# Kernel tuning notes

Hardware: AMD Instinct MI355X
Metric: run time of the kernel (lower is better)

## Reference

```python
import jax, jax.numpy as jnp
import numpy as np

B, T = 1, 1024
V, C, H, L = 50304, 768, 12, 6
K = C // H              # 64, d_head
F = int(C * 3.5) // 32 * 32   # 2688, d_ffn
GN_EPS = 6.4e-4


def _layernorm(x, wb, eps=1e-5):
    mu = x.mean(-1, keepdims=True)
    var = jnp.var(x, axis=-1, keepdims=True)
    return (x - mu) * jax.lax.rsqrt(var + eps) * wb[0] + wb[1]


def _groupnorm(x, wb):  # x: [N, C], groups of size K per head
    xg = x.reshape(-1, H, K)
    mu = xg.mean(-1, keepdims=True)
    var = jnp.var(xg, axis=-1, keepdims=True)
    xg = (xg - mu) * jax.lax.rsqrt(var + GN_EPS)
    return xg.reshape(-1, C) * wb[0] + wb[1]


def _lerp(a, b, w):  # torch.lerp(a, b, w) = a + (b - a) * w
    return a + (b - a) * w


def _shift(x):  # token-shift with zero initial state (fresh LayerState)
    return jnp.concatenate([jnp.zeros_like(x[:, :1]), x[:, :-1]], axis=1)


def _layer(x, p):
    (tm_ln, tm_ts, Wr, Wk, Wv, Wg, Wo, bonus, decay, tm_gn,
     cm_ln, cm_ts, Win, Wout, cWg) = p
    # ---- time mixer ----
    xn = _layernorm(x, tm_ln)
    xp = _shift(xn)
    r = (_lerp(xp, xn, tm_ts[0]) @ Wr).reshape(B, T, H, K)
    k = (_lerp(xp, xn, tm_ts[1]) @ Wk).reshape(B, T, H, K)
    v = (_lerp(xp, xn, tm_ts[2]) @ Wv).reshape(B, T, H, K)
    g = _lerp(xp, xn, tm_ts[3]) @ Wg
    w = jnp.exp(-jnp.exp(decay))  # [H, K] per-channel decay

    def wkv_step(kv, rkv):  # kv: [B,H,K,V]
        r_t, k_t, v_t = rkv  # each [B,H,K]
        a = k_t[..., :, None] * v_t[..., None, :]          # outer product kv_t
        out = jnp.einsum('bhk,bhkv->bhv', r_t, kv + a * bonus[..., None])
        return kv * w[..., None] + a, out

    kv0 = jnp.zeros((B, H, K, K), x.dtype)
    kv_final, out = jax.lax.scan(
        wkv_step, kv0,
        (r.transpose(1, 0, 2, 3), k.transpose(1, 0, 2, 3),
         v.transpose(1, 0, 2, 3)))
    out = out.transpose(1, 0, 2, 3).reshape(B, T, C)
    out = _groupnorm(out.reshape(B * T, C), tm_gn).reshape(B, T, C)
    x = x + (out * jax.nn.silu(g)) @ Wo
    # ---- channel mixer ----
    xn = _layernorm(x, cm_ln)
    xp = _shift(xn)
    h = jnp.square(jax.nn.relu(_lerp(xp, xn, cm_ts[0]) @ Win))
    x = x + (h @ Wout) * jax.nn.sigmoid(_lerp(xp, xn, cm_ts[1]) @ cWg)
    return x, kv_final


def _forward(tokens, embed, embed_ln, tm_ln, tm_ts, tm_Wr, tm_Wk, tm_Wv,
             tm_Wg, tm_Wo, tm_bonus, tm_decay, tm_gn, cm_ln, cm_ts, cm_Win,
             cm_Wout, cm_Wg, head_ln, unembed):
    x = _layernorm(embed[tokens], embed_ln)
    stacked = (tm_ln, tm_ts, tm_Wr, tm_Wk, tm_Wv, tm_Wg, tm_Wo, tm_bonus,
               tm_decay, tm_gn, cm_ln, cm_ts, cm_Win, cm_Wout, cm_Wg)
    x, _ = jax.lax.scan(_layer, x, stacked)  # scan over the L layers
    return _layernorm(x, head_ln) @ unembed  # logits [B, T, V]


def setup_inputs() -> dict:
    key = jax.random.key(0)
    ks = iter(jax.random.split(key, 48))

    def rn(shape, s=0.02):
        return s * jax.random.normal(next(ks), shape, jnp.float32)

    def ln(pre=()):  # stacked (weight, bias) of a LayerNorm/GroupNorm
        return jnp.stack([1.0 + rn(pre + (C,)), rn(pre + (C,))], axis=len(pre))

    return {
        'tokens': jax.random.randint(next(ks), (B, T), 0, V),
        'embed': rn((V, C)),
        'embed_ln': ln(),
        'tm_ln': ln((L,)),
        'tm_ts': jax.random.uniform(next(ks), (L, 4, C), jnp.float32),
        'tm_Wr': rn((L, C, C)),
        'tm_Wk': rn((L, C, C)),
        'tm_Wv': rn((L, C, C)),
        'tm_Wg': rn((L, C, C)),
        'tm_Wo': rn((L, C, C)),
        'tm_bonus': rn((L, H, K), 0.5),
        'tm_decay': rn((L, H, K), 0.5),
        'tm_gn': ln((L,)),
        'cm_ln': ln((L,)),
        'cm_ts': jax.random.uniform(next(ks), (L, 2, C), jnp.float32),
        'cm_Win': rn((L, C, F)),
        'cm_Wout': rn((L, F, C)),
        'cm_Wg': rn((L, C, C)),
        'head_ln': ln(),
        'unembed': rn((C, V)),
    }


def reference(tokens, embed, embed_ln, tm_ln, tm_ts, tm_Wr, tm_Wk, tm_Wv,
              tm_Wg, tm_Wo, tm_bonus, tm_decay, tm_gn, cm_ln, cm_ts, cm_Win,
              cm_Wout, cm_Wg, head_ln, unembed):
    return _forward(tokens, embed, embed_ln, tm_ln, tm_ts, tm_Wr, tm_Wk,
                    tm_Wv, tm_Wg, tm_Wo, tm_bonus, tm_decay, tm_gn, cm_ln,
                    cm_ts, cm_Win, cm_Wout, cm_Wg, head_ln, unembed)
```

## Files before the change

### kernel.cpp

```cpp
#include <hip/hip_runtime.h>
#include <hip/hip_bf16.h>

#define T_LEN 1024
#define CDIM  768
#define HNUM  12
#define KDIM  64
#define LNUM  6
#define FDIM  2688
#define VDIM  50304
#define NCH   16
#define LCH   64

#define WSZ   (CDIM * CDIM)
#define WIN_OFF  (6 * WSZ)
#define WOUT_OFF (WIN_OFF + CDIM * FDIM)
#define WBUF_ELEMS (WOUT_OFF + FDIM * CDIM)

typedef __attribute__((ext_vector_type(4))) float f32x4;
typedef __attribute__((ext_vector_type(8))) short s16x8;

__device__ __forceinline__ ushort f2bf(float f) {
    union { float fv; unsigned u; } v; v.fv = f;
    unsigned r = v.u + 0x7fffu + ((v.u >> 16) & 1u);
    return (ushort)(r >> 16);
}

__device__ __forceinline__ void gload_lds16(const ushort* g, ushort* l) {
    __builtin_amdgcn_global_load_lds(
        (const __attribute__((address_space(1))) void*)g,
        (__attribute__((address_space(3))) void*)l, 16, 0, 0);
}

template <int N_>
__device__ __forceinline__ void wait_vm() {
    if constexpr (N_ == 0)       asm volatile("s_waitcnt vmcnt(0)" ::: "memory");
    else if constexpr (N_ == 6)  asm volatile("s_waitcnt vmcnt(6)" ::: "memory");
    else if constexpr (N_ == 8)  asm volatile("s_waitcnt vmcnt(8)" ::: "memory");
    else if constexpr (N_ == 12) asm volatile("s_waitcnt vmcnt(12)" ::: "memory");
    else                         asm volatile("s_waitcnt vmcnt(16)" ::: "memory");
}
__device__ __forceinline__ void barrier_asm() {
    asm volatile("s_barrier" ::: "memory");
}

__device__ __forceinline__ size_t frag_idx(int nn, int k, int K) {
    int n16 = nn >> 4, ln15 = nn & 15;
    int k64 = k >> 6, s = (k >> 5) & 1, kq = (k >> 3) & 3;
    return ((size_t)(n16 * (K >> 6) + k64) * 2 + s) * 512 + (kq * 16 + ln15) * 8
           + (k & 4);
}

__device__ __forceinline__ void trans_pair(const float* __restrict__ in,
        ushort* __restrict__ out, int R, int C, int tk, int tn0) {
    __shared__ float t0[64][65], t1[64][65];
    int tid = threadIdx.x;
    int r = tid >> 4, c4 = (tid & 15) << 2;
    int k0 = tk << 6, n0 = tn0 << 7, n1 = n0 + 64;
    float4 va[4], vb[4];
    #pragma unroll
    for (int j = 0; j < 4; j++)
        va[j] = *(const float4*)&in[(size_t)(k0 + r + j * 16) * C + n0 + c4];
    #pragma unroll
    for (int j = 0; j < 4; j++)
        vb[j] = *(const float4*)&in[(size_t)(k0 + r + j * 16) * C + n1 + c4];
    #pragma unroll
    for (int j = 0; j < 4; j++) {
        int rr = r + j * 16;
        t0[rr][c4 + 0] = va[j].x; t0[rr][c4 + 1] = va[j].y;
        t0[rr][c4 + 2] = va[j].z; t0[rr][c4 + 3] = va[j].w;
        t1[rr][c4 + 0] = vb[j].x; t1[rr][c4 + 1] = vb[j].y;
        t1[rr][c4 + 2] = vb[j].z; t1[rr][c4 + 3] = vb[j].w;
    }
    __syncthreads();
    #pragma unroll
    for (int j = 0; j < 4; j++) {
        int n = r + j * 16;
        ushort4 u0, u1;
        u0.x = f2bf(t0[c4 + 0][n]); u0.y = f2bf(t0[c4 + 1][n]);
        u0.z = f2bf(t0[c4 + 2][n]); u0.w = f2bf(t0[c4 + 3][n]);
        *(ushort4*)&out[frag_idx(n0 + n, k0 + c4, R)] = u0;
        u1.x = f2bf(t1[c4 + 0][n]); u1.y = f2bf(t1[c4 + 1][n]);
        u1.z = f2bf(t1[c4 + 2][n]); u1.w = f2bf(t1[c4 + 3][n]);
        *(ushort4*)&out[frag_idx(n1 + n, k0 + c4, R)] = u1;
    }
}

__device__ __forceinline__ void trans_tile(const float* __restrict__ in,
        ushort* __restrict__ out, int R, int C, int tk, int tn) {
    __shared__ float tile[64][65];
    int tid = threadIdx.x;
    int r = tid >> 4, c4 = (tid & 15) << 2;
    int k0 = tk << 6, n0 = tn << 6;
    #pragma unroll
    for (int j = 0; j < 4; j++) {
        int rr = r + j * 16;
        float4 f = *(const float4*)&in[(size_t)(k0 + rr) * C + n0 + c4];
        tile[rr][c4 + 0] = f.x; tile[rr][c4 + 1] = f.y;
        tile[rr][c4 + 2] = f.z; tile[rr][c4 + 3] = f.w;
    }
    __syncthreads();
    #pragma unroll
    for (int j = 0; j < 4; j++) {
        int n = r + j * 16;
        ushort4 u;
        u.x = f2bf(tile[c4 + 0][n]);
        u.y = f2bf(tile[c4 + 1][n]);
        u.z = f2bf(tile[c4 + 2][n]);
        u.w = f2bf(tile[c4 + 3][n]);
        *(ushort4*)&out[frag_idx(n0 + n, k0 + c4, R)] = u;
    }
}

__global__ __launch_bounds__(256)
void k_trans(const float* __restrict__ in, ushort* __restrict__ out, int R, int C) {
    trans_tile(in, out, R, C, blockIdx.y, blockIdx.x);
}

__device__ __forceinline__ void conv_layer_pair(int t,
        const float* p0, const float* p1, const float* p2, const float* p3,
        const float* p4, const float* p5, const float* pWin, const float* pWout,
        ushort* wl) {
    const float* in; ushort* out; int R, C, tk, tnp;
    if (t < 432) {
        int mi = t / 72, tt = t % 72;
        switch (mi) {
            case 0: in = p0; break; case 1: in = p1; break;
            case 2: in = p2; break; case 3: in = p3; break;
            case 4: in = p4; break; default: in = p5; break;
        }
        out = wl + (size_t)mi * WSZ; R = 768; C = 768;
        tk = tt / 6; tnp = tt % 6;
    } else if (t < 684) {
        int tt = t - 432;
        in = pWin; out = wl + WIN_OFF; R = 768; C = 2688;
        tk = tt / 21; tnp = tt % 21;
    } else {
        int tt = t - 684;
        in = pWout; out = wl + WOUT_OFF; R = 2688; C = 768;
        tk = tt / 6; tnp = tt % 6;
    }
    trans_pair(in, out, R, C, tk, tnp);
}

__global__ __launch_bounds__(256)
void k_conv_layer(const float* p0, const float* p1, const float* p2,
                  const float* p3, const float* p4, const float* p5,
                  const float* pWin, const float* pWout, ushort* wl) {
    conv_layer_pair(blockIdx.x, p0, p1, p2, p3, p4, p5, pWin, pWout, wl);
}

__global__ __launch_bounds__(256)
void k_conv_all(const float* Wr, const float* Wk, const float* Wv,
                const float* Wg, const float* Wo, const float* Wcg,
                const float* Win, const float* Wout, const float* unemb,
                ushort* wbuf, ushort* ubuf) {
    int b = blockIdx.x;
    if (b < 6 * 936) {
        int l = b / 936, t = b % 936;
        conv_layer_pair(t,
            Wr + (size_t)l * WSZ, Wk + (size_t)l * WSZ, Wv + (size_t)l * WSZ,
            Wg + (size_t)l * WSZ, Wo + (size_t)l * WSZ, Wcg + (size_t)l * WSZ,
            Win + (size_t)l * CDIM * FDIM, Wout + (size_t)l * FDIM * CDIM,
            wbuf + (size_t)l * WBUF_ELEMS);
    } else {
        int t = b - 6 * 936;
        int tk = t / 393, tnp = t % 393;
        trans_pair(unemb, ubuf, CDIM, VDIM, tk, tnp);
    }
}

__global__ __launch_bounds__(256)
void k_ln_bf(const float* __restrict__ x, const float* __restrict__ wb,
             ushort* __restrict__ out) {
    int t = blockIdx.x, tid = threadIdx.x;
    float v[3]; float s = 0.f, s2 = 0.f;
    #pragma unroll
    for (int j = 0; j < 3; j++) {
        v[j] = x[(size_t)t * CDIM + tid + j * 256];
        s += v[j]; s2 += v[j] * v[j];
    }
    #pragma unroll
    for (int m = 32; m; m >>= 1) { s += __shfl_xor(s, m); s2 += __shfl_xor(s2, m); }
    __shared__ float rs[4], rq[4];
    int w = tid >> 6;
    if ((tid & 63) == 0) { rs[w] = s; rq[w] = s2; }
    __syncthreads();
    s = rs[0] + rs[1] + rs[2] + rs[3];
    s2 = rq[0] + rq[1] + rq[2] + rq[3];
    float mu = s * (1.f / CDIM);
    float inv = rsqrtf(s2 * (1.f / CDIM) - mu * mu + 1e-5f);
    #pragma unroll
    for (int j = 0; j < 3; j++) {
        int c = tid + j * 256;
        out[(size_t)t * CDIM + c] = f2bf((v[j] - mu) * inv * wb[c] + wb[CDIM + c]);
    }
}

__global__ __launch_bounds__(256)
void k_embed_ln(const int* __restrict__ tok, const float* __restrict__ embed,
                const float* __restrict__ wb, float* __restrict__ xout) {
    int t = blockIdx.x, tid = threadIdx.x;
    const float* row = embed + (size_t)tok[t] * CDIM;
    float v[3]; float s = 0.f, s2 = 0.f;
    #pragma unroll
    for (int j = 0; j < 3; j++) {
        v[j] = row[tid + j * 256]; s += v[j]; s2 += v[j] * v[j];
    }
    #pragma unroll
    for (int m = 32; m; m >>= 1) { s += __shfl_xor(s, m); s2 += __shfl_xor(s2, m); }
    __shared__ float rs[4], rq[4];
    int w = tid >> 6;
    if ((tid & 63) == 0) { rs[w] = s; rq[w] = s2; }
    __syncthreads();
    s = rs[0] + rs[1] + rs[2] + rs[3];
    s2 = rq[0] + rq[1] + rq[2] + rq[3];
    float mu = s * (1.f / CDIM);
    float inv = rsqrtf(s2 * (1.f / CDIM) - mu * mu + 1e-5f);
    #pragma unroll
    for (int j = 0; j < 3; j++) {
        int c = tid + j * 256;
        xout[(size_t)t * CDIM + c] = (v[j] - mu) * inv * wb[c] + wb[CDIM + c];
    }
}

template <int NM>
__global__ __launch_bounds__(256)
void k_lnlerp(const float* __restrict__ x, const float* __restrict__ lnw,
              const float* __restrict__ ts, ushort* __restrict__ mix) {
    int t = blockIdx.x, tid = threadIdx.x;
    bool has = (t > 0);
    float vb[3], va[3];
    float sb = 0.f, qb = 0.f, sa = 0.f, qa = 0.f;
    #pragma unroll
    for (int j = 0; j < 3; j++) {
        int c = tid + j * 256;
        vb[j] = x[(size_t)t * CDIM + c];
        sb += vb[j]; qb += vb[j] * vb[j];
        va[j] = has ? x[(size_t)(t - 1) * CDIM + c] : 0.f;
        sa += va[j]; qa += va[j] * va[j];
    }
    #pragma unroll
    for (int m = 32; m; m >>= 1) {
        sb += __shfl_xor(sb, m); qb += __shfl_xor(qb, m);
        sa += __shfl_xor(sa, m); qa += __shfl_xor(qa, m);
    }
    __shared__ float r0[4], r1[4], r2[4], r3[4];
    int w = tid >> 6;
    if ((tid & 63) == 0) { r0[w] = sb; r1[w] = qb; r2[w] = sa; r3[w] = qa; }
    __syncthreads();
    sb = r0[0] + r0[1] + r0[2] + r0[3]; qb = r1[0] + r1[1] + r1[2] + r1[3];
    sa = r2[0] + r2[1] + r2[2] + r2[3]; qa = r3[0] + r3[1] + r3[2] + r3[3];
    float mub = sb * (1.f / CDIM);
    float invb = rsqrtf(qb * (1.f / CDIM) - mub * mub + 1e-5f);
    float mua = sa * (1.f / CDIM);
    float inva = rsqrtf(qa * (1.f / CDIM) - mua * mua + 1e-5f);
    #pragma unroll
    for (int j = 0; j < 3; j++) {
        int c = tid + j * 256;
        float wgt = lnw[c], bia = lnw[CDIM + c];
        float xb = (vb[j] - mub) * invb * wgt + bia;
        float xa = has ? (va[j] - mua) * inva * wgt + bia : 0.f;
        #pragma unroll
        for (int m = 0; m < NM; m++) {
            float tv = ts[m * CDIM + c];
            mix[((size_t)m * T_LEN + t) * CDIM + c] = f2bf(xa + (xb - xa) * tv);
        }
    }
}

template <int BM, int BN, int EPI>
__device__ __forceinline__ void gemm_body(
        const ushort* __restrict__ A, const ushort* __restrict__ Bf,
        float* __restrict__ Cf, ushort* __restrict__ Cb,
        const float* __restrict__ resid, const float* __restrict__ gate,
        int N, int K, int mb, int nb, ushort* Al) {
    const int tid = threadIdx.x, lane = tid & 63, wave = tid >> 6;
    constexpr int WM = BM / 2, WN = BN / 2, FM = WM / 16, FN = WN / 16;
    const int wm = (wave >> 1) * WM, wn = (wave & 1) * WN;
    constexpr int AR = BM / 32;
    constexpr int LD = AR + 2 * FN;
    const int kq = lane >> 4, ln15 = lane & 15;

    const size_t bstride = (size_t)(K >> 6) * 2048;
    const char* bbase = (const char*)Bf +
        (size_t)((nb + wn) >> 4) * bstride + lane * 16;

    auto stageA = [&](int buf, int kt) {
        int k0 = kt << 6;
        #pragma unroll
        for (int r = 0; r < AR; r++) {
            int slot = tid + r * 256;
            int row = slot >> 3, g = slot & 7;
            int gk = ((g ^ (row & 7)) << 3);
            gload_lds16(A + (size_t)(mb + row) * K + k0 + gk,
                        &Al[buf * BM * 64 + slot * 8]);
        }
    };
    auto loadB = [&](s16x8 (&dst)[2][FN], int kt) {
        const char* p = bbase + (size_t)kt * 2048;
        #pragma unroll
        for (int s = 0; s < 2; s++)
            #pragma unroll
            for (int j = 0; j < FN; j++)
                dst[s][j] = *(const s16x8*)(p + (size_t)j * bstride + s * 1024);
    };

    f32x4 acc[FM][FN];
    #pragma unroll
    for (int i = 0; i < FM; i++)
        #pragma unroll
        for (int j = 0; j < FN; j++) acc[i][j] = (f32x4)0.f;

    auto compute = [&](const ushort* Ab, s16x8 (&bfr)[2][FN]) {
        #pragma unroll
        for (int s = 0; s < 2; s++) {
            s16x8 af[FM];
            #pragma unroll
            for (int i = 0; i < FM; i++) {
                int row = wm + i * 16 + ln15;
                int g = (s * 4 + kq) ^ (row & 7);
                af[i] = *(const s16x8*)&Ab[row * 64 + g * 8];
            }
            #pragma unroll
            for (int i = 0; i < FM; i++)
                #pragma unroll
                for (int j = 0; j < FN; j++)
                    acc[i][j] = __builtin_amdgcn_mfma_f32_16x16x32_bf16(
                        af[i], bfr[s][j], acc[i][j], 0, 0, 0);
        }
    };

    const int nt = K >> 6;
    s16x8 b0[2][FN], b1[2][FN];
    stageA(0, 0); loadB(b0, 0);
    stageA(1, 1); loadB(b1, 1);
    for (int t = 0; t < nt; t += 2) {
        wait_vm<LD>();
        barrier_asm();
        compute(Al, b0);
        barrier_asm();
        if (t + 2 < nt) { stageA(0, t + 2); loadB(b0, t + 2); }
        if (t + 2 < nt) wait_vm<LD>();
        else            wait_vm<0>();
        barrier_asm();
        compute(Al + BM * 64, b1);
        barrier_asm();
        if (t + 3 < nt) { stageA(1, t + 3); loadB(b1, t + 3); }
    }
    #pragma unroll
    for (int i = 0; i < FM; i++) {
        int rbase = mb + wm + i * 16 + (lane >> 4) * 4;
        #pragma unroll
        for (int j = 0; j < FN; j++) {
            int col = nb + wn + j * 16 + (lane & 15);
            #pragma unroll
            for (int r = 0; r < 4; r++) {
                size_t idx = (size_t)(rbase + r) * N + col;
                float vv = acc[i][j][r];
                if constexpr (EPI == 0) {
                    Cf[idx] = vv;
                } else if constexpr (EPI == 1) {
                    Cf[idx] = resid[idx] + vv;
                } else if constexpr (EPI == 2) {
                    float z = vv > 0.f ? vv * vv : 0.f;
                    Cb[idx] = f2bf(z);
                } else {
                    float gv = gate[idx];
                    Cf[idx] = resid[idx] + vv / (1.f + __expf(-gv));
                }
            }
        }
    }
}

template <int BM, int BN, int EPI, bool BATCH>
__global__ __launch_bounds__(256)
void k_gemm_std(const ushort* __restrict__ A, const ushort* __restrict__ Bf,
                float* __restrict__ Cf, ushort* __restrict__ Cb,
                const float* __restrict__ resid, const float* __restrict__ gate,
                int N, int K) {
    __shared__ __align__(16) ushort Al[2 * BM * 64];
    if constexpr (BATCH) {
        int z = blockIdx.z;
        A  += (size_t)z * T_LEN * CDIM;
        Bf += (size_t)z * CDIM * CDIM;
        Cf += (size_t)z * T_LEN * CDIM;
    }
    gemm_body<BM, BN, EPI>(A, Bf, Cf, Cb, resid, gate, N, K,
                           blockIdx.y * BM, blockIdx.x * BN, Al);
}

__global__ __launch_bounds__(256)
void k_gemm_head(const ushort* __restrict__ A, const ushort* __restrict__ Bf,
                 float* __restrict__ C) {
    __shared__ __align__(16) ushort Al[2 * 128 * 64];
    int id = blockIdx.x;
    int xcd = id & 7, slot = id >> 3;
    int mb = slot & 7, nbl = slot >> 3;
    int nb = nbl * 8 + xcd;
    if (nb >= VDIM / 128) return;
    gemm_body<128, 128, 0>(A, Bf, C, nullptr, nullptr, nullptr,
                           VDIM, CDIM, mb * 128, nb * 128, Al);
}

__global__ __launch_bounds__(256)
void k_cmix(const ushort* __restrict__ mix, const ushort* __restrict__ wl,
            ushort* __restrict__ hb, float* __restrict__ gcm) {
    __shared__ __align__(16) ushort Al[2 * 128 * 64];
    int bx = blockIdx.x, mb = blockIdx.y * 128;
    if (bx < FDIM / 64) {
        gemm_body<128, 64, 2>(mix, wl + WIN_OFF, nullptr, hb, nullptr, nullptr,
                              FDIM, CDIM, mb, bx * 64, Al);
    } else {
        gemm_body<128, 64, 0>(mix + (size_t)T_LEN * CDIM, wl + 5 * WSZ, gcm,
                              nullptr, nullptr, nullptr, CDIM, CDIM, mb,
                              (bx - FDIM / 64) * 64, Al);
    }
}

__global__ __launch_bounds__(256)
void k_wkv1(const float* __restrict__ kb, const float* __restrict__ vb,
            const float* __restrict__ decay, float* __restrict__ Stil) {
    int c = blockIdx.x / HNUM, h = blockIdx.x % HNUM;
    __shared__ float kl[4096], vl[4096], wsh[64];
    int tid = threadIdx.x;
    for (int idx = tid; idx < 4096; idx += 256) {
        int j = idx >> 6, cc = idx & 63;
        size_t g = (size_t)(c * LCH + j) * CDIM + h * 64 + cc;
        kl[idx] = kb[g]; vl[idx] = vb[g];
    }
    if (tid < 64) wsh[tid] = expf(-expf(decay[h * 64 + tid]));
    __syncthreads();
    int k = tid >> 2, v0 = (tid & 3) * 16;
    float w = wsh[k], f = 1.f;
    float s[16];
    #pragma unroll
    for (int i = 0; i < 16; i++) s[i] = 0.f;
    for (int j = 63; j >= 0; --j) {
        float kw = kl[j * 64 + k] * f;
        #pragma unroll
        for (int i = 0; i < 16; i++) s[i] += kw * vl[j * 64 + v0 + i];
        f *= w;
    }
    float* dst = Stil + ((size_t)(c * HNUM + h) << 12) + k * 64 + v0;
    #pragma unroll
    for (int i = 0; i < 16; i++) dst[i] = s[i];
}

__global__ __launch_bounds__(256)
void k_wkv23(const float* __restrict__ rb, const float* __restrict__ kb,
             const float* __restrict__ vb, const float* __restrict__ Stil,
             const float* __restrict__ decay, const float* __restrict__ bonus,
             const float* __restrict__ gate, const float* __restrict__ gnw,
             ushort* __restrict__ y) {
    int c = blockIdx.x / HNUM, h = blockIdx.x % HNUM;
    __shared__ float rl[4096], kl[4096], vl[4096];
    __shared__ float part[4][4096];
    __shared__ float wsh[64], bsh[64];
    int tid = threadIdx.x;
    for (int idx = tid; idx < 4096; idx += 256) {
        int j = idx >> 6, cc = idx & 63;
        size_t g = (size_t)(c * LCH + j) * CDIM + h * 64 + cc;
        rl[idx] = rb[g]; kl[idx] = kb[g]; vl[idx] = vb[g];
    }
    if (tid < 64) {
        wsh[tid] = expf(-expf(decay[h * 64 + tid]));
        bsh[tid] = bonus[h * 64 + tid];
    }
    __syncthreads();
    int v = tid & 63, kg = tid >> 6;
    float S[16], wr[16], br[16], w64[16];
    #pragma unroll
    for (int i = 0; i < 16; i++) {
        S[i] = 0.f;
        wr[i] = wsh[kg * 16 + i];
        br[i] = bsh[kg * 16 + i];
        float t2 = wr[i];
        t2 *= t2; t2 *= t2; t2 *= t2; t2 *= t2; t2 *= t2; t2 *= t2;
        w64[i] = t2;
    }
    for (int cc = 0; cc < c; cc++) {
        const float* sp = Stil + ((size_t)(cc * HNUM + h) << 12);
        #pragma unroll
        for (int i = 0; i < 16; i++)
            S[i] = S[i] * w64[i] + sp[(kg * 16 + i) * 64 + v];
    }
    for (int j = 0; j < 64; j++) {
        float vj = vl[j * 64 + v];
        const float4* kp = (const float4*)&kl[j * 64 + kg * 16];
        const float4* rp = (const float4*)&rl[j * 64 + kg * 16];
        float rsum = 0.f;
        #pragma unroll
        for (int qq = 0; qq < 4; qq++) {
            float4 k4 = kp[qq], r4 = rp[qq];
            const float* kf = (const float*)&k4;
            const float* rf = (const float*)&r4;
            #pragma unroll
            for (int e = 0; e < 4; e++) {
                int i = qq * 4 + e;
                float a = kf[e] * vj;
                rsum += rf[e] * (S[i] + a * br[i]);
                S[i] = S[i] * wr[i] + a;
            }
        }
        part[kg][j * 64 + v] = rsum;
    }
    __syncthreads();
    for (int jj = 0; jj < 16; jj++) {
        int j = kg * 16 + jj;
        float o = part[0][j * 64 + v] + part[1][j * 64 + v] +
                  part[2][j * 64 + v] + part[3][j * 64 + v];
        float s = o, s2 = o * o;
        #pragma unroll
        for (int m = 32; m; m >>= 1) { s += __shfl_xor(s, m); s2 += __shfl_xor(s2, m); }
        float mu = s * (1.f / 64.f);
        float var = s2 * (1.f / 64.f) - mu * mu;
        float xg = (o - mu) * rsqrtf(var + 6.4e-4f);
        int t = c * LCH + j, col = h * 64 + v;
        float gv = gate[(size_t)t * CDIM + col];
        float silu = gv / (1.f + __expf(-gv));
        y[(size_t)t * CDIM + col] = f2bf((xg * gnw[col] + gnw[CDIM + col]) * silu);
    }
}

extern "C" void kernel_launch(void* const* d_in, const int* in_sizes, int n_in,
                              void* d_out, int out_size, void* d_ws, size_t ws_size,
                              hipStream_t stream) {
    const int*   tok      = (const int*)d_in[0];
    const float* embed    = (const float*)d_in[1];
    const float* embed_ln = (const float*)d_in[2];
    const float* tm_ln    = (const float*)d_in[3];
    const float* tm_ts    = (const float*)d_in[4];
    const float* tm_Wr    = (const float*)d_in[5];
    const float* tm_Wk    = (const float*)d_in[6];
    const float* tm_Wv    = (const float*)d_in[7];
    const float* tm_Wg    = (const float*)d_in[8];
    const float* tm_Wo    = (const float*)d_in[9];
    const float* tm_bonus = (const float*)d_in[10];
    const float* tm_decay = (const float*)d_in[11];
    const float* tm_gn    = (const float*)d_in[12];
    const float* cm_ln    = (const float*)d_in[13];
    const float* cm_ts    = (const float*)d_in[14];
    const float* cm_Win   = (const float*)d_in[15];
    const float* cm_Wout  = (const float*)d_in[16];
    const float* cm_Wg    = (const float*)d_in[17];
    const float* head_ln  = (const float*)d_in[18];
    const float* unembed  = (const float*)d_in[19];
    float* out = (float*)d_out;

    const size_t TC = (size_t)T_LEN * CDIM;
    char* wp = (char*)d_ws;
    auto alloc = [&](size_t bytes) {
        char* p = wp; wp += (bytes + 255) & ~(size_t)255; return p;
    };
    float*  x    = (float*)alloc(TC * 4);
    ushort* mix  = (ushort*)alloc(4 * TC * 2);
    float*  rkvg = (float*)alloc(4 * TC * 4);
    float*  gcm  = (float*)alloc(TC * 4);
    ushort* y    = (ushort*)alloc(TC * 2);
    ushort* hb   = (ushort*)alloc((size_t)T_LEN * FDIM * 2);
    float*  Stil = (float*)alloc((size_t)NCH * HNUM * 4096 * 4);
    ushort* ubuf = (ushort*)alloc((size_t)CDIM * VDIM * 2);
    size_t fixed_bytes = (size_t)(wp - (char*)d_ws);
    const size_t per_layer = ((size_t)WBUF_ELEMS * 2 + 255) & ~(size_t)255;
    bool all6 = (fixed_bytes + 6 * per_layer) <= ws_size;
    ushort* wbuf = (ushort*)alloc(all6 ? 6 * per_layer : per_layer);
    if ((size_t)(wp - (char*)d_ws) > ws_size) return;

    if (all6) {
        k_conv_all<<<6 * 936 + 4716, 256, 0, stream>>>(
            tm_Wr, tm_Wk, tm_Wv, tm_Wg, tm_Wo, cm_Wg, cm_Win, cm_Wout,
            unembed, wbuf, ubuf);
    } else {
        k_trans<<<dim3(VDIM / 64, CDIM / 64), 256, 0, stream>>>(
            unembed, ubuf, CDIM, VDIM);
    }
    k_embed_ln<<<T_LEN, 256, 0, stream>>>(tok, embed, embed_ln, x);

    dim3 g64(CDIM / 64, T_LEN / 64);
    dim3 gQKVG(CDIM / 64, T_LEN / 128, 4);
    dim3 gCmix(FDIM / 64 + CDIM / 64, T_LEN / 128);

    for (int l = 0; l < LNUM; l++) {
        ushort* wl = all6 ? (ushort*)((char*)wbuf + (size_t)l * per_layer) : wbuf;
        if (!all6) {
            const size_t lo = (size_t)l * CDIM * CDIM;
            k_conv_layer<<<936, 256, 0, stream>>>(
                tm_Wr + lo, tm_Wk + lo, tm_Wv + lo, tm_Wg + lo, tm_Wo + lo,
                cm_Wg + lo, cm_Win + (size_t)l * CDIM * FDIM,
                cm_Wout + (size_t)l * FDIM * CDIM, wl);
        }
        const float* dec = tm_decay + (size_t)l * HNUM * KDIM;
        const float* bon = tm_bonus + (size_t)l * HNUM * KDIM;

        k_lnlerp<4><<<T_LEN, 256, 0, stream>>>(x, tm_ln + (size_t)l * 2 * CDIM,
                                               tm_ts + (size_t)l * 4 * CDIM, mix);
        k_gemm_std<128,64,0,true><<<gQKVG, 256, 0, stream>>>(
            mix, wl, rkvg, nullptr, nullptr, nullptr, CDIM, CDIM);
        k_wkv1<<<NCH * HNUM, 256, 0, stream>>>(rkvg + TC, rkvg + 2 * TC, dec, Stil);
        k_wkv23<<<NCH * HNUM, 256, 0, stream>>>(rkvg, rkvg + TC, rkvg + 2 * TC,
            Stil, dec, bon, rkvg + 3 * TC, tm_gn + (size_t)l * 2 * CDIM, y);
        k_gemm_std<64,64,1,false><<<g64, 256, 0, stream>>>(
            y, wl + 4 * WSZ, x, nullptr, x, nullptr, CDIM, CDIM);

        k_lnlerp<2><<<T_LEN, 256, 0, stream>>>(x, cm_ln + (size_t)l * 2 * CDIM,
                                               cm_ts + (size_t)l * 2 * CDIM, mix);
        k_cmix<<<gCmix, 256, 0, stream>>>(mix, wl, hb, gcm);
        k_gemm_std<64,64,3,false><<<g64, 256, 0, stream>>>(
            hb, wl + WOUT_OFF, x, nullptr, x, gcm, CDIM, FDIM);
    }

    k_ln_bf<<<T_LEN, 256, 0, stream>>>(x, head_ln, mix);
    k_gemm_head<<<3200, 256, 0, stream>>>(mix, ubuf, out);
}
```

Measured before the change: 893.0 us.

## Transpose weights in 128x128 quads, fuse embed LN into conversion, custom head GEMM

Weight conversion blocks now each transpose four 64x64 tiles (128x128) instead of two, halving the block count and putting more loads in flight per block. The embedding layernorm is folded into the conversion kernel as extra blocks, removing one launch. The vocabulary head GEMM gets a dedicated inline body that stages B fragments through LDS with double buffering instead of the generic gemm_body. The cost is higher LDS use per conversion block (about 66KB), which lowers occupancy.

```diff
diff --git a/kernel.cpp b/kernel.cpp
--- a/kernel.cpp
+++ b/kernel.cpp
@@ -50,39 +50,48 @@
            + (k & 4);
 }
 
-__device__ __forceinline__ void trans_pair(const float* __restrict__ in,
-        ushort* __restrict__ out, int R, int C, int tk, int tn0) {
-    __shared__ float t0[64][65], t1[64][65];
+__device__ __forceinline__ void trans_quad(const float* __restrict__ in,
+        ushort* __restrict__ out, int R, int C, int tkq, int tnp) {
+    __shared__ float tl[2][2][64][65];
     int tid = threadIdx.x;
     int r = tid >> 4, c4 = (tid & 15) << 2;
-    int k0 = tk << 6, n0 = tn0 << 7, n1 = n0 + 64;
-    float4 va[4], vb[4];
-    #pragma unroll
-    for (int j = 0; j < 4; j++)
-        va[j] = *(const float4*)&in[(size_t)(k0 + r + j * 16) * C + n0 + c4];
-    #pragma unroll
-    for (int j = 0; j < 4; j++)
-        vb[j] = *(const float4*)&in[(size_t)(k0 + r + j * 16) * C + n1 + c4];
-    #pragma unroll
-    for (int j = 0; j < 4; j++) {
-        int rr = r + j * 16;
-        t0[rr][c4 + 0] = va[j].x; t0[rr][c4 + 1] = va[j].y;
-        t0[rr][c4 + 2] = va[j].z; t0[rr][c4 + 3] = va[j].w;
-        t1[rr][c4 + 0] = vb[j].x; t1[rr][c4 + 1] = vb[j].y;
-        t1[rr][c4 + 2] = vb[j].z; t1[rr][c4 + 3] = vb[j].w;
-    }
+    int k0 = tkq << 7, n0 = tnp << 7;
+    float4 v[2][2][4];
+    #pragma unroll
+    for (int dk = 0; dk < 2; dk++)
+        #pragma unroll
+        for (int dn = 0; dn < 2; dn++)
+            #pragma unroll
+            for (int j = 0; j < 4; j++)
+                v[dk][dn][j] = *(const float4*)
+                    &in[(size_t)(k0 + dk * 64 + r + j * 16) * C + n0 + dn * 64 + c4];
+    #pragma unroll
+    for (int dk = 0; dk < 2; dk++)
+        #pragma unroll
+        for (int dn = 0; dn < 2; dn++)
+            #pragma unroll
+            for (int j = 0; j < 4; j++) {
+                int rr = r + j * 16;
+                tl[dk][dn][rr][c4 + 0] = v[dk][dn][j].x;
+                tl[dk][dn][rr][c4 + 1] = v[dk][dn][j].y;
+                tl[dk][dn][rr][c4 + 2] = v[dk][dn][j].z;
+                tl[dk][dn][rr][c4 + 3] = v[dk][dn][j].w;
+            }
     __syncthreads();
     #pragma unroll
-    for (int j = 0; j < 4; j++) {
-        int n = r + j * 16;
-        ushort4 u0, u1;
-        u0.x = f2bf(t0[c4 + 0][n]); u0.y = f2bf(t0[c4 + 1][n]);
-        u0.z = f2bf(t0[c4 + 2][n]); u0.w = f2bf(t0[c4 + 3][n]);
-        *(ushort4*)&out[frag_idx(n0 + n, k0 + c4, R)] = u0;
-        u1.x = f2bf(t1[c4 + 0][n]); u1.y = f2bf(t1[c4 + 1][n]);
-        u1.z = f2bf(t1[c4 + 2][n]); u1.w = f2bf(t1[c4 + 3][n]);
-        *(ushort4*)&out[frag_idx(n1 + n, k0 + c4, R)] = u1;
-    }
+    for (int dk = 0; dk < 2; dk++)
+        #pragma unroll
+        for (int dn = 0; dn < 2; dn++)
+            #pragma unroll
+            for (int j = 0; j < 4; j++) {
+                int n = r + j * 16;
+                ushort4 u;
+                u.x = f2bf(tl[dk][dn][c4 + 0][n]);
+                u.y = f2bf(tl[dk][dn][c4 + 1][n]);
+                u.z = f2bf(tl[dk][dn][c4 + 2][n]);
+                u.w = f2bf(tl[dk][dn][c4 + 3][n]);
+                *(ushort4*)&out[frag_idx(n0 + dn * 64 + n, k0 + dk * 64 + c4, R)] = u;
+            }
 }
 
 __device__ __forceinline__ void trans_tile(const float* __restrict__ in,
@@ -116,68 +125,15 @@
     trans_tile(in, out, R, C, blockIdx.y, blockIdx.x);
 }
 
-__device__ __forceinline__ void conv_layer_pair(int t,
-        const float* p0, const float* p1, const float* p2, const float* p3,
-        const float* p4, const float* p5, const float* pWin, const float* pWout,
-        ushort* wl) {
-    const float* in; ushort* out; int R, C, tk, tnp;
-    if (t < 432) {
-        int mi = t / 72, tt = t % 72;
-        switch (mi) {
-            case 0: in = p0; break; case 1: in = p1; break;
-            case 2: in = p2; break; case 3: in = p3; break;
-            case 4: in = p4; break; default: in = p5; break;
-        }
-        out = wl + (size_t)mi * WSZ; R = 768; C = 768;
-        tk = tt / 6; tnp = tt % 6;
-    } else if (t < 684) {
-        int tt = t - 432;
-        in = pWin; out = wl + WIN_OFF; R = 768; C = 2688;
-        tk = tt / 21; tnp = tt % 21;
-    } else {
-        int tt = t - 684;
-        in = pWout; out = wl + WOUT_OFF; R = 2688; C = 768;
-        tk = tt / 6; tnp = tt % 6;
-    }
-    trans_pair(in, out, R, C, tk, tnp);
-}
-
-__global__ __launch_bounds__(256)
-void k_conv_layer(const float* p0, const float* p1, const float* p2,
-                  const float* p3, const float* p4, const float* p5,
-                  const float* pWin, const float* pWout, ushort* wl) {
-    conv_layer_pair(blockIdx.x, p0, p1, p2, p3, p4, p5, pWin, pWout, wl);
-}
-
-__global__ __launch_bounds__(256)
-void k_conv_all(const float* Wr, const float* Wk, const float* Wv,
-                const float* Wg, const float* Wo, const float* Wcg,
-                const float* Win, const float* Wout, const float* unemb,
-                ushort* wbuf, ushort* ubuf) {
-    int b = blockIdx.x;
-    if (b < 6 * 936) {
-        int l = b / 936, t = b % 936;
-        conv_layer_pair(t,
-            Wr + (size_t)l * WSZ, Wk + (size_t)l * WSZ, Wv + (size_t)l * WSZ,
-            Wg + (size_t)l * WSZ, Wo + (size_t)l * WSZ, Wcg + (size_t)l * WSZ,
-            Win + (size_t)l * CDIM * FDIM, Wout + (size_t)l * FDIM * CDIM,
-            wbuf + (size_t)l * WBUF_ELEMS);
-    } else {
-        int t = b - 6 * 936;
-        int tk = t / 393, tnp = t % 393;
-        trans_pair(unemb, ubuf, CDIM, VDIM, tk, tnp);
-    }
-}
-
-__global__ __launch_bounds__(256)
-void k_ln_bf(const float* __restrict__ x, const float* __restrict__ wb,
-             ushort* __restrict__ out) {
-    int t = blockIdx.x, tid = threadIdx.x;
+__device__ __forceinline__ void embed_ln_row(int t, const int* __restrict__ tok,
+        const float* __restrict__ embed, const float* __restrict__ wb,
+        float* __restrict__ xout) {
+    int tid = threadIdx.x;
+    const float* row = embed + (size_t)tok[t] * CDIM;
     float v[3]; float s = 0.f, s2 = 0.f;
     #pragma unroll
     for (int j = 0; j < 3; j++) {
-        v[j] = x[(size_t)t * CDIM + tid + j * 256];
-        s += v[j]; s2 += v[j] * v[j];
+        v[j] = row[tid + j * 256]; s += v[j]; s2 += v[j] * v[j];
     }
     #pragma unroll
     for (int m = 32; m; m >>= 1) { s += __shfl_xor(s, m); s2 += __shfl_xor(s2, m); }
@@ -192,19 +148,101 @@
     #pragma unroll
     for (int j = 0; j < 3; j++) {
         int c = tid + j * 256;
-        out[(size_t)t * CDIM + c] = f2bf((v[j] - mu) * inv * wb[c] + wb[CDIM + c]);
+        xout[(size_t)t * CDIM + c] = (v[j] - mu) * inv * wb[c] + wb[CDIM + c];
     }
 }
 
 __global__ __launch_bounds__(256)
 void k_embed_ln(const int* __restrict__ tok, const float* __restrict__ embed,
                 const float* __restrict__ wb, float* __restrict__ xout) {
+    embed_ln_row(blockIdx.x, tok, embed, wb, xout);
+}
+
+__device__ __forceinline__ void conv_layer_quad(int t,
+        const float* p0, const float* p1, const float* p2, const float* p3,
+        const float* p4, const float* p5, const float* pWin, const float* pWout,
+        ushort* wl) {
+    const float* in; ushort* out; int R, C, tkq, tnp;
+    if (t < 216) {
+        int mi = t / 36, tt = t % 36;
+        switch (mi) {
+            case 0: in = p0; break; case 1: in = p1; break;
+            case 2: in = p2; break; case 3: in = p3; break;
+            case 4: in = p4; break; default: in = p5; break;
+        }
+        out = wl + (size_t)mi * WSZ; R = 768; C = 768;
+        tkq = tt / 6; tnp = tt % 6;
+    } else if (t < 342) {
+        int tt = t - 216;
+        in = pWin; out = wl + WIN_OFF; R = 768; C = 2688;
+        tkq = tt / 21; tnp = tt % 21;
+    } else {
+        int tt = t - 342;
+        in = pWout; out = wl + WOUT_OFF; R = 2688; C = 768;
+        tkq = tt / 6; tnp = tt % 6;
+    }
+    trans_quad(in, out, R, C, tkq, tnp);
+}
+
+__global__ __launch_bounds__(256)
+void k_conv_layer(const float* p0, const float* p1, const float* p2,
+                  const float* p3, const float* p4, const float* p5,
+                  const float* pWin, const float* pWout, ushort* wl) {
+    int t = blockIdx.x;
+    const float* in; ushort* out; int R, C, tk, tn;
+    if (t < 864) {
+        int mi = t / 144, tt = t % 144;
+        switch (mi) {
+            case 0: in = p0; break; case 1: in = p1; break;
+            case 2: in = p2; break; case 3: in = p3; break;
+            case 4: in = p4; break; default: in = p5; break;
+        }
+        out = wl + (size_t)mi * WSZ; R = 768; C = 768;
+        tk = tt / 12; tn = tt % 12;
+    } else if (t < 1368) {
+        int tt = t - 864;
+        in = pWin; out = wl + WIN_OFF; R = 768; C = 2688;
+        tk = tt / 42; tn = tt % 42;
+    } else {
+        int tt = t - 1368;
+        in = pWout; out = wl + WOUT_OFF; R = 2688; C = 768;
+        tk = tt / 12; tn = tt % 12;
+    }
+    trans_tile(in, out, R, C, tk, tn);
+}
+
+__global__ __launch_bounds__(256)
+void k_conv_all(const float* Wr, const float* Wk, const float* Wv,
+                const float* Wg, const float* Wo, const float* Wcg,
+                const float* Win, const float* Wout, const float* unemb,
+                ushort* wbuf, ushort* ubuf,
+                const int* tok, const float* embed, const float* eln, float* x) {
+    int b = blockIdx.x;
+    if (b < 6 * 468) {
+        int l = b / 468, t = b % 468;
+        conv_layer_quad(t,
+            Wr + (size_t)l * WSZ, Wk + (size_t)l * WSZ, Wv + (size_t)l * WSZ,
+            Wg + (size_t)l * WSZ, Wo + (size_t)l * WSZ, Wcg + (size_t)l * WSZ,
+            Win + (size_t)l * CDIM * FDIM, Wout + (size_t)l * FDIM * CDIM,
+            wbuf + (size_t)l * WBUF_ELEMS);
+    } else if (b < 6 * 468 + 2358) {
+        int t = b - 6 * 468;
+        int tkq = t / 393, tnp = t % 393;
+        trans_quad(unemb, ubuf, CDIM, VDIM, tkq, tnp);
+    } else {
+        embed_ln_row(b - (6 * 468 + 2358), tok, embed, eln, x);
+    }
+}
+
+__global__ __launch_bounds__(256)
+void k_ln_bf(const float* __restrict__ x, const float* __restrict__ wb,
+             ushort* __restrict__ out) {
     int t = blockIdx.x, tid = threadIdx.x;
-    const float* row = embed + (size_t)tok[t] * CDIM;
     float v[3]; float s = 0.f, s2 = 0.f;
     #pragma unroll
     for (int j = 0; j < 3; j++) {
-        v[j] = row[tid + j * 256]; s += v[j]; s2 += v[j] * v[j];
+        v[j] = x[(size_t)t * CDIM + tid + j * 256];
+        s += v[j]; s2 += v[j] * v[j];
     }
     #pragma unroll
     for (int m = 32; m; m >>= 1) { s += __shfl_xor(s, m); s2 += __shfl_xor(s2, m); }
@@ -219,7 +257,7 @@
     #pragma unroll
     for (int j = 0; j < 3; j++) {
         int c = tid + j * 256;
-        xout[(size_t)t * CDIM + c] = (v[j] - mu) * inv * wb[c] + wb[CDIM + c];
+        out[(size_t)t * CDIM + c] = f2bf((v[j] - mu) * inv * wb[c] + wb[CDIM + c]);
     }
 }
 
@@ -394,13 +432,89 @@
 void k_gemm_head(const ushort* __restrict__ A, const ushort* __restrict__ Bf,
                  float* __restrict__ C) {
     __shared__ __align__(16) ushort Al[2 * 128 * 64];
+    __shared__ __align__(16) ushort Bl[2 * 128 * 64];
     int id = blockIdx.x;
     int xcd = id & 7, slot = id >> 3;
-    int mb = slot & 7, nbl = slot >> 3;
-    int nb = nbl * 8 + xcd;
-    if (nb >= VDIM / 128) return;
-    gemm_body<128, 128, 0>(A, Bf, C, nullptr, nullptr, nullptr,
-                           VDIM, CDIM, mb * 128, nb * 128, Al);
+    int mbi = slot & 7, nbl = slot >> 3;
+    int nbi = nbl * 8 + xcd;
+    if (nbi >= VDIM / 128) return;
+    const int mb = mbi * 128, nb = nbi * 128;
+    const int tid = threadIdx.x, lane = tid & 63, wave = tid >> 6;
+    const int wm = (wave >> 1) * 64, wn = (wave & 1) * 64;
+    const int kq = lane >> 4, ln15 = lane & 15;
+    constexpr int K = CDIM, N = VDIM;
+    const size_t bstride = (size_t)(K >> 6) * 1024;
+
+    auto stage = [&](int buf, int kt) {
+        int k0 = kt << 6;
+        #pragma unroll
+        for (int r = 0; r < 4; r++) {
+            int slot2 = tid + r * 256;
+            int row = slot2 >> 3, g = slot2 & 7;
+            int gk = ((g ^ (row & 7)) << 3);
+            gload_lds16(A + (size_t)(mb + row) * K + k0 + gk,
+                        &Al[buf * 8192 + slot2 * 8]);
+        }
+        #pragma unroll
+        for (int r = 0; r < 4; r++) {
+            int slot2 = tid + r * 256;
+            int n16 = slot2 >> 7, off = slot2 & 127;
+            gload_lds16(Bf + (size_t)((nb >> 4) + n16) * bstride
+                           + (size_t)kt * 1024 + off * 8,
+                        &Bl[buf * 8192 + slot2 * 8]);
+        }
+    };
+
+    f32x4 acc[4][4];
+    #pragma unroll
+    for (int i = 0; i < 4; i++)
+        #pragma unroll
+        for (int j = 0; j < 4; j++) acc[i][j] = (f32x4)0.f;
+
+    stage(0, 0);
+    stage(1, 1);
+    for (int t = 0; t < 12; t++) {
+        if (t < 11) wait_vm<8>();
+        else        wait_vm<0>();
+        barrier_asm();
+        const ushort* Ab = &Al[(t & 1) * 8192];
+        const ushort* Bb = &Bl[(t & 1) * 8192];
+        #pragma unroll
+        for (int s = 0; s < 2; s++) {
+            s16x8 af[4], bfr[4];
+            #pragma unroll
+            for (int i = 0; i < 4; i++) {
+                int row = wm + i * 16 + ln15;
+                int g = (s * 4 + kq) ^ (row & 7);
+                af[i] = *(const s16x8*)&Ab[row * 64 + g * 8];
+            }
+            #pragma unroll
+            for (int j = 0; j < 4; j++) {
+                int n16 = (wn >> 4) + j;
+                bfr[j] = *(const s16x8*)&Bl[(t & 1) * 8192 + n16 * 1024
+                                            + (s * 512) + lane * 8];
+            }
+            #pragma unroll
+            for (int i = 0; i < 4; i++)
+                #pragma unroll
+                for (int j = 0; j < 4; j++)
+                    acc[i][j] = __builtin_amdgcn_mfma_f32_16x16x32_bf16(
+                        af[i], bfr[j], acc[i][j], 0, 0, 0);
+        }
+        barrier_asm();
+        if (t + 2 < 12) stage(t & 1, t + 2);
+    }
+    #pragma unroll
+    for (int i = 0; i < 4; i++) {
+        int rbase = mb + wm + i * 16 + (lane >> 4) * 4;
+        #pragma unroll
+        for (int j = 0; j < 4; j++) {
+            int col = nb + wn + j * 16 + ln15;
+            #pragma unroll
+            for (int r = 0; r < 4; r++)
+                C[(size_t)(rbase + r) * N + col] = acc[i][j][r];
+        }
+    }
 }
 
 __global__ __launch_bounds__(256)
@@ -568,14 +682,14 @@
     if ((size_t)(wp - (char*)d_ws) > ws_size) return;
 
     if (all6) {
-        k_conv_all<<<6 * 936 + 4716, 256, 0, stream>>>(
+        k_conv_all<<<6 * 468 + 2358 + 1024, 256, 0, stream>>>(
             tm_Wr, tm_Wk, tm_Wv, tm_Wg, tm_Wo, cm_Wg, cm_Win, cm_Wout,
-            unembed, wbuf, ubuf);
+            unembed, wbuf, ubuf, tok, embed, embed_ln, x);
     } else {
         k_trans<<<dim3(VDIM / 64, CDIM / 64), 256, 0, stream>>>(
             unembed, ubuf, CDIM, VDIM);
-    }
-    k_embed_ln<<<T_LEN, 256, 0, stream>>>(tok, embed, embed_ln, x);
+        k_embed_ln<<<T_LEN, 256, 0, stream>>>(tok, embed, embed_ln, x);
+    }
 
     dim3 g64(CDIM / 64, T_LEN / 64);
     dim3 gQKVG(CDIM / 64, T_LEN / 128, 4);
@@ -585,7 +699,7 @@
         ushort* wl = all6 ? (ushort*)((char*)wbuf + (size_t)l * per_layer) : wbuf;
         if (!all6) {
             const size_t lo = (size_t)l * CDIM * CDIM;
-            k_conv_layer<<<936, 256, 0, stream>>>(
+            k_conv_layer<<<1872, 256, 0, stream>>>(
                 tm_Wr + lo, tm_Wk + lo, tm_Wv + lo, tm_Wg + lo, tm_Wo + lo,
                 cm_Wg + lo, cm_Win + (size_t)l * CDIM * FDIM,
                 cm_Wout + (size_t)l * FDIM * CDIM, wl);
```

New measurement: 875.2 us. 2.0% less time.
